# Optimization experiments

Hardware: AMD Instinct MI355X
Metric: run time of the kernel (lower is better)

Reference implementation:

```python
import jax, jax.numpy as jnp
import numpy as np

FEW, BATCH, D, STEPS = 128, 4096, 512, 4


def setup_inputs() -> dict:
    key = jax.random.key(0)
    ks = jax.random.split(key, 6)
    H = 2 * D  # LSTMCell hidden size
    return {
        "support": jax.random.normal(ks[0], (FEW, D), jnp.float32),
        "query": jax.random.normal(ks[1], (BATCH, D), jnp.float32),
        "W_ih": jax.random.normal(ks[2], (4 * H, D), jnp.float32) * (1.0 / np.sqrt(H)),
        "W_hh": jax.random.normal(ks[3], (4 * H, H), jnp.float32) * (1.0 / np.sqrt(H)),
        "b_ih": jax.random.normal(ks[4], (4 * H,), jnp.float32) * 0.01,
        "b_hh": jax.random.normal(ks[5], (4 * H,), jnp.float32) * 0.01,
        "process_step": STEPS,
    }


def reference(support, query, W_ih, W_hh, b_ih, b_hh, process_step):
    # support: (few, d); query: (batch, d); LSTMCell hidden = 2d.
    d = query.shape[1]
    batch = query.shape[0]
    h_r = jnp.zeros((batch, 2 * d), query.dtype)
    c = jnp.zeros((batch, 2 * d), query.dtype)
    h = query
    for _ in range(process_step):
        # PyTorch LSTMCell: gates ordered (i, f, g, o)
        gates = query @ W_ih.T + b_ih + h_r @ W_hh.T + b_hh  # (batch, 8d)
        i, f, g, o = jnp.split(gates, 4, axis=1)
        c = jax.nn.sigmoid(f) * c + jax.nn.sigmoid(i) * jnp.tanh(g)
        h_r_ = jax.nn.sigmoid(o) * jnp.tanh(c)  # (batch, 2d)
        h = query + h_r_[:, :d]  # (batch, d)
        attn = jax.nn.softmax(h @ support.T, axis=1)  # (batch, few)
        r = attn @ support  # (batch, d)
        h_r = jnp.concatenate([h, r], axis=1)  # (batch, 2d)
    return h
```

## Files before the change

### kernel.cpp

```cpp
#include <hip/hip_runtime.h>

#define BATCH 4096
#define DDIM  512
#define FEWN  128
#define LDA1  640
#define GATEN 2048
#define CDIM  512

typedef unsigned short ushort_t;
typedef __attribute__((ext_vector_type(8))) short bf16x8;
typedef __attribute__((ext_vector_type(4))) float f32x4;

__device__ inline ushort_t f2bf(float f) {
  unsigned u = __float_as_uint(f);
  unsigned r = (u + 0x7FFFu + ((u >> 16) & 1u)) >> 16;
  return (ushort_t)r;
}
__device__ inline float bf2f(ushort_t h) { return __uint_as_float((unsigned)h << 16); }
__device__ inline float bf2f_u(unsigned h16) { return __uint_as_float(h16 << 16); }

__device__ inline float sigmoidf(float x) { return 1.f / (1.f + __expf(-x)); }
__device__ inline float tanh_fast(float x) {
  float ax = fabsf(x);
  float t = __expf(-2.f * ax);
  float r = (1.f - t) / (1.f + t);
  return copysignf(r, x);
}

__device__ inline int orig_row(int colp) {
  return ((colp >> 4) & 3) * 1024 + ((colp >> 6) << 4) + (colp & 15);
}

__device__ inline void async_copy16(ushort_t* lds, const ushort_t* g) {
  __builtin_amdgcn_global_load_lds(
      (const __attribute__((address_space(1))) unsigned int*)g,
      (__attribute__((address_space(3))) unsigned int*)lds, 16, 0, 0);
}

#define XCD_SWZ()                                                            \
  int bx = blockIdx.x, by = blockIdx.y;                                      \
  {                                                                          \
    const int gx = gridDim.x;                                                \
    const int id = by * gx + bx;                                             \
    if ((gx & 7) == 0) {                                                     \
      const int cpx = gx >> 3;                                               \
      const int x = id & 7, s = id >> 3;                                     \
      bx = x * cpx + (s % cpx);                                              \
      by = s / cpx;                                                          \
    } else {                                                                 \
      const int nwg = gx * gridDim.y;                                        \
      const int qq = nwg >> 3, rr = nwg & 7;                                 \
      const int x = id & 7, s = id >> 3;                                     \
      const int nid = (x < rr ? x * (qq + 1) : rr * (qq + 1) + (x - rr) * qq) + s; \
      bx = nid % gx; by = nid / gx;                                          \
    }                                                                        \
  }

#define STAGE8(dA, dB, kk)                                                   \
    async_copy16(dA,              gA0 + (kk));                               \
    async_copy16(dA + 512,        gA0 + (size_t)16 * lda + (kk));            \
    async_copy16(dA + 4096,       gA0 + (kk) + 32);                          \
    async_copy16(dA + 4096 + 512, gA0 + (size_t)16 * lda + (kk) + 32);       \
    async_copy16(dB,              gB0 + (kk));                               \
    async_copy16(dB + 512,        gB0 + (size_t)16 * ldb + (kk));            \
    async_copy16(dB + 4096,       gB0 + (kk) + 32);                          \
    async_copy16(dB + 4096 + 512, gB0 + (size_t)16 * ldb + (kk) + 32);

#define KLOOP_DBUF()                                                         \
  const int nIter = K >> 6;                                                  \
  { STAGE8(sA, sB, 0) }                                                      \
  if (nIter > 1) { STAGE8(sA + 8192, sB + 8192, 64) }                        \
  for (int kt = 0; kt < nIter; ++kt) {                                       \
    if (kt + 1 < nIter) asm volatile("s_waitcnt vmcnt(8)" ::: "memory");     \
    else                asm volatile("s_waitcnt vmcnt(0)" ::: "memory");     \
    __builtin_amdgcn_s_barrier();                                            \
    const int cur = (kt & 1) * 8192;                                         \
    _Pragma("unroll")                                                        \
    for (int h = 0; h < 2; ++h) {                                            \
      bf16x8 af[4], bfr[4];                                                  \
      _Pragma("unroll")                                                      \
      for (int mi = 0; mi < 4; ++mi)                                         \
        af[mi] = *(const bf16x8*)&lA[cur + h * 4096 + (wr * 64 + mi * 16 + lr) * 32 + kg * 8]; \
      _Pragma("unroll")                                                      \
      for (int ni = 0; ni < 4; ++ni)                                         \
        bfr[ni] = *(const bf16x8*)&lB[cur + h * 4096 + (wc * 64 + ni * 16 + lr) * 32 + kg * 8]; \
      _Pragma("unroll")                                                      \
      for (int mi = 0; mi < 4; ++mi)                                         \
        _Pragma("unroll")                                                    \
        for (int ni = 0; ni < 4; ++ni)                                       \
          acc[mi][ni] = __builtin_amdgcn_mfma_f32_16x16x32_bf16(af[mi], bfr[ni], acc[mi][ni], 0, 0, 0); \
    }                                                                        \
    __builtin_amdgcn_s_barrier();                                            \
    if (kt + 2 < nIter) {                                                    \
      const int k2 = (kt + 2) << 6;                                          \
      STAGE8(sA + cur, sB + cur, k2)                                         \
    }                                                                        \
  }

#define GEMM_PROLOG()                                                        \
  __shared__ __align__(16) ushort_t lA[2 * 8192];                            \
  __shared__ __align__(16) ushort_t lB[2 * 8192];                            \
  const int tid = threadIdx.x;                                               \
  const int wid = tid >> 6, lane = tid & 63;                                 \
  const int wr = wid >> 1, wc = wid & 1;                                     \
  XCD_SWZ()                                                                  \
  const int m0 = by * 128, n0 = bx * 128;                                    \
  const int lr = lane & 15, kg = lane >> 4;                                  \
  f32x4 acc[4][4] = {};                                                      \
  const int srow = lane >> 2;                                                \
  const int scol = (lane & 3) * 8;                                           \
  const ushort_t* gA0 = A + (size_t)(m0 + wid * 32 + srow) * lda + scol;     \
  const ushort_t* gB0 = B + (size_t)(n0 + wid * 32 + srow) * ldb + scol;     \
  ushort_t* sA = &lA[wid * 1024];                                            \
  ushort_t* sB = &lB[wid * 1024];                                            \
  KLOOP_DBUF()

__launch_bounds__(256)
__global__ void gemm_wide(const ushort_t* __restrict__ A, const ushort_t* __restrict__ B,
                          ushort_t* __restrict__ gbase, ushort_t* __restrict__ c,
                          ushort_t* __restrict__ A1out, ushort_t* __restrict__ A2out,
                          const float* __restrict__ b1, const float* __restrict__ b2,
                          int K, int lda, int ldb) {
  GEMM_PROLOG()
  if (n0 < 2048) {
    const int jj = ((n0 + wc * 64) >> 6) * 16 + lr;
    const float bi0 = b1[jj]        + b2[jj];
    const float bi2 = b1[2048 + jj] + b2[2048 + jj];
    const float bi3 = b1[3072 + jj] + b2[3072 + jj];
#pragma unroll
    for (int mi = 0; mi < 4; ++mi) {
#pragma unroll
      for (int r = 0; r < 4; ++r) {
        const int row = m0 + wr * 64 + mi * 16 + kg * 4 + r;
        const float si = sigmoidf(acc[mi][0][r] + bi0);
        const float tg = tanh_fast(acc[mi][2][r] + bi2);
        const float so = sigmoidf(acc[mi][3][r] + bi3);
        const float cn = si * tg;
        c[(size_t)row * CDIM + jj] = f2bf(cn);
        const float hr = so * tanh_fast(cn);
        const ushort_t hi = f2bf(hr);
        const ushort_t lo = f2bf(hr - bf2f(hi));
        A1out[(size_t)row * LDA1 + jj] = hi;
        A2out[(size_t)row * DDIM + jj] = lo;
      }
    }
  } else {
    const int jj = ((n0 - 2048 + wc * 64) >> 6) * 16 + lr;
    const float bi0 = b1[jj]        + b2[jj];
    const float bi1 = b1[1024 + jj] + b2[1024 + jj];
    const float bi2 = b1[2048 + jj] + b2[2048 + jj];
    const float bi3 = b1[3072 + jj] + b2[3072 + jj];
#pragma unroll
    for (int mi = 0; mi < 4; ++mi)
#pragma unroll
      for (int r = 0; r < 4; ++r) {
        const int row = m0 + wr * 64 + mi * 16 + kg * 4 + r;
        uint2 p;
        p.x = (unsigned)f2bf(acc[mi][0][r] + bi0) | ((unsigned)f2bf(acc[mi][1][r] + bi1) << 16);
        p.y = (unsigned)f2bf(acc[mi][2][r] + bi2) | ((unsigned)f2bf(acc[mi][3][r] + bi3) << 16);
        *(uint2*)&gbase[(size_t)row * GATEN + jj * 4] = p;
      }
  }
}

template<int MODE>
__launch_bounds__(256)
__global__ void gemm_fused(const ushort_t* __restrict__ A, const ushort_t* __restrict__ B,
                           const ushort_t* __restrict__ base, ushort_t* __restrict__ c,
                           ushort_t* __restrict__ A1out, ushort_t* __restrict__ A2out,
                           const float* __restrict__ query, float* __restrict__ out,
                           int K, int lda, int ldb) {
  GEMM_PROLOG()
  const int jj = ((n0 + wc * 64) >> 6) * 16 + lr;
#pragma unroll
  for (int mi = 0; mi < 4; ++mi) {
#pragma unroll
    for (int r = 0; r < 4; ++r) {
      const int row = m0 + wr * 64 + mi * 16 + kg * 4 + r;
      const uint2 p = *(const uint2*)&base[(size_t)row * GATEN + jj * 4];
      const float g0 = bf2f_u(p.x & 0xFFFFu) + acc[mi][0][r];
      const float g1 = bf2f_u(p.x >> 16)     + acc[mi][1][r];
      const float g2 = bf2f_u(p.y & 0xFFFFu) + acc[mi][2][r];
      const float g3 = bf2f_u(p.y >> 16)     + acc[mi][3][r];
      const float si = sigmoidf(g0);
      const float sf = sigmoidf(g1);
      const float tg = tanh_fast(g2);
      const float so = sigmoidf(g3);
      const size_t ci = (size_t)row * CDIM + jj;
      const float cn = sf * bf2f(c[ci]) + si * tg;
      if (MODE != 2) c[ci] = f2bf(cn);
      const float hr = so * tanh_fast(cn);
      if (MODE == 2) {
        out[(size_t)row * DDIM + jj] = query[(size_t)row * DDIM + jj] + hr;
      } else {
        const ushort_t hi = f2bf(hr);
        const ushort_t lo = f2bf(hr - bf2f(hi));
        A1out[(size_t)row * LDA1 + jj] = hi;
        A2out[(size_t)row * DDIM + jj] = lo;
      }
    }
  }
}

__launch_bounds__(256)
__global__ void gemm_splitk6(const ushort_t* __restrict__ A1, const ushort_t* __restrict__ A2,
                             int lda1, int lda2,
                             const ushort_t* __restrict__ Bc, float* __restrict__ Cf) {
  __shared__ __align__(16) ushort_t lA[2 * 8192];
  __shared__ __align__(16) ushort_t lB[2 * 8192];
  const int tid = threadIdx.x;
  const int wid = tid >> 6, lane = tid & 63;
  const int wr = wid >> 1, wc = wid & 1;
  const int seg = blockIdx.x >> 1;
  const int koff = (blockIdx.x & 1) * 256;
  const int m0 = blockIdx.y * 128;
  const int lr = lane & 15, kg = lane >> 4;
  f32x4 acc[4][4] = {};
  const int srow = lane >> 2;
  const int scol = (lane & 3) * 8;
  const ushort_t* A = (seg == 1) ? A2 : A1;
  const int lda = (seg == 1) ? lda2 : lda1;
  const int ldb = 1536;
  const ushort_t* gA0 = A + (size_t)(m0 + wid * 32 + srow) * lda + koff + scol;
  const ushort_t* gB0 = Bc + (size_t)(wid * 32 + srow) * 1536 + seg * 512 + koff + scol;
  ushort_t* sA = &lA[wid * 1024];
  ushort_t* sB = &lB[wid * 1024];
  const int K = 256;
  KLOOP_DBUF()
#pragma unroll
  for (int mi = 0; mi < 4; ++mi)
#pragma unroll
    for (int ni = 0; ni < 4; ++ni)
#pragma unroll
      for (int r = 0; r < 4; ++r) {
        const int row = m0 + wr * 64 + mi * 16 + kg * 4 + r;
        const int col = wc * 64 + ni * 16 + lr;
        atomicAdd(&Cf[(size_t)row * FEWN + col], acc[mi][ni][r]);
      }
}

template<int EPI>
__launch_bounds__(256)
__global__ void gemm_bt(const ushort_t* __restrict__ A, const ushort_t* __restrict__ B,
                        float* __restrict__ Cf, ushort_t* __restrict__ Cb,
                        int K, int lda, int ldb, int ldc) {
  GEMM_PROLOG()
#pragma unroll
  for (int mi = 0; mi < 4; ++mi)
#pragma unroll
    for (int ni = 0; ni < 4; ++ni)
#pragma unroll
      for (int r = 0; r < 4; ++r) {
        const int row = m0 + wr * 64 + mi * 16 + kg * 4 + r;
        const int col = n0 + wc * 64 + ni * 16 + lr;
        const float v = acc[mi][ni][r];
        const size_t o = (size_t)row * ldc + col;
        if (EPI == 2) Cb[o] = f2bf(v);
        else          Cf[o] = v;
      }
}

__global__ void softmax_kernel(const float* __restrict__ logits, const float* __restrict__ baseL,
                               ushort_t* __restrict__ A1) {
  const int row = blockIdx.x * 4 + (threadIdx.x >> 6);
  const int lane = threadIdx.x & 63;
  const size_t ro = (size_t)row * FEWN;
  const float x0 = logits[ro + lane]      + baseL[ro + lane];
  const float x1 = logits[ro + 64 + lane] + baseL[ro + 64 + lane];
  float m = fmaxf(x0, x1);
#pragma unroll
  for (int s = 32; s > 0; s >>= 1) m = fmaxf(m, __shfl_xor(m, s));
  const float e0 = __expf(x0 - m), e1 = __expf(x1 - m);
  float sum = e0 + e1;
#pragma unroll
  for (int s = 32; s > 0; s >>= 1) sum += __shfl_xor(sum, s);
  const float inv = 1.f / sum;
  A1[(size_t)row * LDA1 + 512 + lane]      = f2bf(e0 * inv);
  A1[(size_t)row * LDA1 + 512 + 64 + lane] = f2bf(e1 * inv);
}

__global__ void setup_all(const float* __restrict__ Wih, const float* __restrict__ Whh,
                          const float* __restrict__ q, const float* __restrict__ s,
                          ushort_t* __restrict__ wcomb, ushort_t* __restrict__ B2,
                          ushort_t* __restrict__ whhRP, ushort_t* __restrict__ Q_cat,
                          ushort_t* __restrict__ B_cat) {
  const int b = blockIdx.x;
  const int tid = threadIdx.x;
  if (b < 8192) {
    const int idx = b * 256 + tid;
    const int r = idx >> 9, cc = idx & 511;
    ushort_t v;
    if (r < 2048) {
      v = f2bf(Wih[(size_t)orig_row(r) * 512 + cc]);
    } else {
      const int og = orig_row(r - 2048);
      v = f2bf(Wih[(size_t)og * 512 + cc] + Whh[(size_t)og * 1024 + cc]);
    }
    wcomb[idx] = v;
  } else if (b < 16384) {
    const int idx = (b - 8192) * 256 + tid;
    const int r = idx >> 10, k = idx & 1023;
    const ushort_t v = f2bf(Whh[(size_t)orig_row(r) * 1024 + k]);
    if (k < 512) B2[(size_t)r * LDA1 + k] = v;
    else         whhRP[(size_t)r * 512 + (k - 512)] = v;
  } else if (b < 24576) {
    const int idx = (b - 16384) * 256 + tid;
    const int bb = idx >> 9, cc = idx & 511;
    const float v = q[idx];
    const ushort_t hi = f2bf(v);
    const ushort_t lo = f2bf(v - bf2f(hi));
    const size_t ro = (size_t)bb * 1536;
    Q_cat[ro + cc] = hi;
    Q_cat[ro + 512 + cc] = lo;
    Q_cat[ro + 1024 + cc] = hi;
  } else {
    const int idx = (b - 24576) * 256 + tid;
    const int n = idx >> 9, cc = idx & 511;
    const float v = s[idx];
    const ushort_t hi = f2bf(v);
    const ushort_t lo = f2bf(v - bf2f(hi));
    const size_t ro = (size_t)n * 1536;
    B_cat[ro + cc] = hi;
    B_cat[ro + 512 + cc] = hi;
    B_cat[ro + 1024 + cc] = lo;
  }
}

extern "C" void kernel_launch(void* const* d_in, const int* in_sizes, int n_in,
                              void* d_out, int out_size, void* d_ws, size_t ws_size,
                              hipStream_t stream) {
  const float* support = (const float*)d_in[0];
  const float* query   = (const float*)d_in[1];
  const float* W_ih    = (const float*)d_in[2];
  const float* W_hh    = (const float*)d_in[3];
  const float* b_ih    = (const float*)d_in[4];
  const float* b_hh    = (const float*)d_in[5];
  float* out = (float*)d_out;

  char* ws = (char*)d_ws;
  size_t off = 0;
  auto alloc = [&](size_t bytes) { char* p = ws + off; off += (bytes + 255) & ~255ull; return p; };
  ushort_t* gates_baseP = (ushort_t*)alloc((size_t)BATCH * GATEN * 2);
  ushort_t* cbuf        = (ushort_t*)alloc((size_t)BATCH * CDIM * 2);
  ushort_t* A1a         = (ushort_t*)alloc((size_t)BATCH * LDA1 * 2);
  ushort_t* A1b         = (ushort_t*)alloc((size_t)BATCH * LDA1 * 2);
  ushort_t* A2a         = (ushort_t*)alloc((size_t)BATCH * DDIM * 2);
  ushort_t* A2b         = (ushort_t*)alloc((size_t)BATCH * DDIM * 2);
  ushort_t* Q_cat       = (ushort_t*)alloc((size_t)BATCH * 1536 * 2);
  ushort_t* wcomb       = (ushort_t*)alloc((size_t)4096 * 512 * 2);
  ushort_t* B2          = (ushort_t*)alloc((size_t)GATEN * LDA1 * 2);
  ushort_t* whhRP       = (ushort_t*)alloc((size_t)GATEN * 512 * 2);
  ushort_t* B_cat       = (ushort_t*)alloc((size_t)FEWN * 1536 * 2);
  const size_t LOFS = (size_t)BATCH * FEWN;
  float*    logits3     = (float*)   alloc(3 * LOFS * 4);
  float*    lgBase      = (float*)   alloc(LOFS * 4);
  const size_t zbytes = 4 * LOFS * 4;

  const dim3 blk(256);

  setup_all<<<24832, blk, 0, stream>>>(W_ih, W_hh, query, support,
                                       wcomb, B2, whhRP, Q_cat, B_cat);
  hipMemsetAsync(logits3, 0, zbytes, stream);

  gemm_splitk6<<<dim3(6, 32), blk, 0, stream>>>(
      Q_cat, Q_cat + 512, 1536, 1536, B_cat, lgBase);

  gemm_bt<2><<<dim3(1, 16), blk, 0, stream>>>(whhRP, B_cat, nullptr, B2 + 512,
                                              512, 512, 1536, LDA1);

  gemm_wide<<<dim3(32, 32), blk, 0, stream>>>(
      Q_cat, wcomb, gates_baseP, cbuf, A1a, A2a, b_ih, b_hh, 512, 1536, 512);

  auto attn_phase = [&](int s, ushort_t* A1, ushort_t* A2) {
    float* lg = logits3 + (size_t)s * LOFS;
    gemm_splitk6<<<dim3(6, 32), blk, 0, stream>>>(A1, A2, LDA1, DDIM, B_cat, lg);
    softmax_kernel<<<BATCH / 4, blk, 0, stream>>>(lg, lgBase, A1);
  };

  attn_phase(0, A1a, A2a);

  gemm_fused<1><<<dim3(16, 32), blk, 0, stream>>>(
      A1a, B2, gates_baseP, cbuf, A1b, A2b, nullptr, nullptr, 640, LDA1, LDA1);
  attn_phase(1, A1b, A2b);

  gemm_fused<1><<<dim3(16, 32), blk, 0, stream>>>(
      A1b, B2, gates_baseP, cbuf, A1a, A2a, nullptr, nullptr, 640, LDA1, LDA1);
  attn_phase(2, A1a, A2a);

  gemm_fused<2><<<dim3(16, 32), blk, 0, stream>>>(
      A1a, B2, gates_baseP, cbuf, nullptr, nullptr, query, out, 640, LDA1, LDA1);
}
```

Measured before the change: 189.8 us.

## Merge prologue GEMMs into one launch and fold memset into setup kernel

Three independent prologue GEMMs (base-logit split-K, W_hh·support projection, wide gate GEMM with LSTM epilogue) are combined into a single kernel that dispatches on block index, and the hipMemsetAsync zeroing of the logits buffers is moved into extra blocks of the setup kernel. This is meant to remove launch overhead and the tail-idle gaps between small kernels, letting the small GEMMs run alongside the large one. The zeroing count matches 4*LOFS floats as float4 stores. The shared macro prologue is refactored into a device helper plus a common tile macro.

```diff
diff --git a/kernel.cpp b/kernel.cpp
--- a/kernel.cpp
+++ b/kernel.cpp
@@ -37,24 +37,20 @@
       (__attribute__((address_space(3))) unsigned int*)lds, 16, 0, 0);
 }
 
-#define XCD_SWZ()                                                            \
-  int bx = blockIdx.x, by = blockIdx.y;                                      \
-  {                                                                          \
-    const int gx = gridDim.x;                                                \
-    const int id = by * gx + bx;                                             \
-    if ((gx & 7) == 0) {                                                     \
-      const int cpx = gx >> 3;                                               \
-      const int x = id & 7, s = id >> 3;                                     \
-      bx = x * cpx + (s % cpx);                                              \
-      by = s / cpx;                                                          \
-    } else {                                                                 \
-      const int nwg = gx * gridDim.y;                                        \
-      const int qq = nwg >> 3, rr = nwg & 7;                                 \
-      const int x = id & 7, s = id >> 3;                                     \
-      const int nid = (x < rr ? x * (qq + 1) : rr * (qq + 1) + (x - rr) * qq) + s; \
-      bx = nid % gx; by = nid / gx;                                          \
-    }                                                                        \
+__device__ inline void xcd_map(int gx, int gy, int id, int& bx, int& by) {
+  if ((gx & 7) == 0) {
+    const int cpx = gx >> 3;
+    const int x = id & 7, s = id >> 3;
+    bx = x * cpx + (s % cpx);
+    by = s / cpx;
+  } else {
+    const int nwg = gx * gy;
+    const int qq = nwg >> 3, rr = nwg & 7;
+    const int x = id & 7, s = id >> 3;
+    const int nid = (x < rr ? x * (qq + 1) : rr * (qq + 1) + (x - rr) * qq) + s;
+    bx = nid % gx; by = nid / gx;
   }
+}
 
 #define STAGE8(dA, dB, kk)                                                   \
     async_copy16(dA,              gA0 + (kk));                               \
@@ -97,71 +93,18 @@
     }                                                                        \
   }
 
-#define GEMM_PROLOG()                                                        \
+#define TILE_COMMON()                                                        \
   __shared__ __align__(16) ushort_t lA[2 * 8192];                            \
   __shared__ __align__(16) ushort_t lB[2 * 8192];                            \
   const int tid = threadIdx.x;                                               \
   const int wid = tid >> 6, lane = tid & 63;                                 \
   const int wr = wid >> 1, wc = wid & 1;                                     \
-  XCD_SWZ()                                                                  \
-  const int m0 = by * 128, n0 = bx * 128;                                    \
   const int lr = lane & 15, kg = lane >> 4;                                  \
-  f32x4 acc[4][4] = {};                                                      \
   const int srow = lane >> 2;                                                \
   const int scol = (lane & 3) * 8;                                           \
-  const ushort_t* gA0 = A + (size_t)(m0 + wid * 32 + srow) * lda + scol;     \
-  const ushort_t* gB0 = B + (size_t)(n0 + wid * 32 + srow) * ldb + scol;     \
+  f32x4 acc[4][4] = {};                                                      \
   ushort_t* sA = &lA[wid * 1024];                                            \
-  ushort_t* sB = &lB[wid * 1024];                                            \
-  KLOOP_DBUF()
-
-__launch_bounds__(256)
-__global__ void gemm_wide(const ushort_t* __restrict__ A, const ushort_t* __restrict__ B,
-                          ushort_t* __restrict__ gbase, ushort_t* __restrict__ c,
-                          ushort_t* __restrict__ A1out, ushort_t* __restrict__ A2out,
-                          const float* __restrict__ b1, const float* __restrict__ b2,
-                          int K, int lda, int ldb) {
-  GEMM_PROLOG()
-  if (n0 < 2048) {
-    const int jj = ((n0 + wc * 64) >> 6) * 16 + lr;
-    const float bi0 = b1[jj]        + b2[jj];
-    const float bi2 = b1[2048 + jj] + b2[2048 + jj];
-    const float bi3 = b1[3072 + jj] + b2[3072 + jj];
-#pragma unroll
-    for (int mi = 0; mi < 4; ++mi) {
-#pragma unroll
-      for (int r = 0; r < 4; ++r) {
-        const int row = m0 + wr * 64 + mi * 16 + kg * 4 + r;
-        const float si = sigmoidf(acc[mi][0][r] + bi0);
-        const float tg = tanh_fast(acc[mi][2][r] + bi2);
-        const float so = sigmoidf(acc[mi][3][r] + bi3);
-        const float cn = si * tg;
-        c[(size_t)row * CDIM + jj] = f2bf(cn);
-        const float hr = so * tanh_fast(cn);
-        const ushort_t hi = f2bf(hr);
-        const ushort_t lo = f2bf(hr - bf2f(hi));
-        A1out[(size_t)row * LDA1 + jj] = hi;
-        A2out[(size_t)row * DDIM + jj] = lo;
-      }
-    }
-  } else {
-    const int jj = ((n0 - 2048 + wc * 64) >> 6) * 16 + lr;
-    const float bi0 = b1[jj]        + b2[jj];
-    const float bi1 = b1[1024 + jj] + b2[1024 + jj];
-    const float bi2 = b1[2048 + jj] + b2[2048 + jj];
-    const float bi3 = b1[3072 + jj] + b2[3072 + jj];
-#pragma unroll
-    for (int mi = 0; mi < 4; ++mi)
-#pragma unroll
-      for (int r = 0; r < 4; ++r) {
-        const int row = m0 + wr * 64 + mi * 16 + kg * 4 + r;
-        uint2 p;
-        p.x = (unsigned)f2bf(acc[mi][0][r] + bi0) | ((unsigned)f2bf(acc[mi][1][r] + bi1) << 16);
-        p.y = (unsigned)f2bf(acc[mi][2][r] + bi2) | ((unsigned)f2bf(acc[mi][3][r] + bi3) << 16);
-        *(uint2*)&gbase[(size_t)row * GATEN + jj * 4] = p;
-      }
-  }
-}
+  ushort_t* sB = &lB[wid * 1024];
 
 template<int MODE>
 __launch_bounds__(256)
@@ -170,7 +113,13 @@
                            ushort_t* __restrict__ A1out, ushort_t* __restrict__ A2out,
                            const float* __restrict__ query, float* __restrict__ out,
                            int K, int lda, int ldb) {
-  GEMM_PROLOG()
+  TILE_COMMON()
+  int bx, by;
+  xcd_map(gridDim.x, gridDim.y, blockIdx.y * gridDim.x + blockIdx.x, bx, by);
+  const int m0 = by * 128, n0 = bx * 128;
+  const ushort_t* gA0 = A + (size_t)(m0 + wid * 32 + srow) * lda + scol;
+  const ushort_t* gB0 = B + (size_t)(n0 + wid * 32 + srow) * ldb + scol;
+  KLOOP_DBUF()
   const int jj = ((n0 + wc * 64) >> 6) * 16 + lr;
 #pragma unroll
   for (int mi = 0; mi < 4; ++mi) {
@@ -206,25 +155,15 @@
 __global__ void gemm_splitk6(const ushort_t* __restrict__ A1, const ushort_t* __restrict__ A2,
                              int lda1, int lda2,
                              const ushort_t* __restrict__ Bc, float* __restrict__ Cf) {
-  __shared__ __align__(16) ushort_t lA[2 * 8192];
-  __shared__ __align__(16) ushort_t lB[2 * 8192];
-  const int tid = threadIdx.x;
-  const int wid = tid >> 6, lane = tid & 63;
-  const int wr = wid >> 1, wc = wid & 1;
+  TILE_COMMON()
   const int seg = blockIdx.x >> 1;
   const int koff = (blockIdx.x & 1) * 256;
   const int m0 = blockIdx.y * 128;
-  const int lr = lane & 15, kg = lane >> 4;
-  f32x4 acc[4][4] = {};
-  const int srow = lane >> 2;
-  const int scol = (lane & 3) * 8;
   const ushort_t* A = (seg == 1) ? A2 : A1;
   const int lda = (seg == 1) ? lda2 : lda1;
   const int ldb = 1536;
   const ushort_t* gA0 = A + (size_t)(m0 + wid * 32 + srow) * lda + koff + scol;
   const ushort_t* gB0 = Bc + (size_t)(wid * 32 + srow) * 1536 + seg * 512 + koff + scol;
-  ushort_t* sA = &lA[wid * 1024];
-  ushort_t* sB = &lB[wid * 1024];
   const int K = 256;
   KLOOP_DBUF()
 #pragma unroll
@@ -239,25 +178,102 @@
       }
 }
 
-template<int EPI>
 __launch_bounds__(256)
-__global__ void gemm_bt(const ushort_t* __restrict__ A, const ushort_t* __restrict__ B,
-                        float* __restrict__ Cf, ushort_t* __restrict__ Cb,
-                        int K, int lda, int ldb, int ldc) {
-  GEMM_PROLOG()
-#pragma unroll
-  for (int mi = 0; mi < 4; ++mi)
-#pragma unroll
-    for (int ni = 0; ni < 4; ++ni)
-#pragma unroll
-      for (int r = 0; r < 4; ++r) {
-        const int row = m0 + wr * 64 + mi * 16 + kg * 4 + r;
-        const int col = n0 + wc * 64 + ni * 16 + lr;
-        const float v = acc[mi][ni][r];
-        const size_t o = (size_t)row * ldc + col;
-        if (EPI == 2) Cb[o] = f2bf(v);
-        else          Cf[o] = v;
+__global__ void prologue_mega(const ushort_t* __restrict__ Qcat, const ushort_t* __restrict__ Bcat,
+                              const ushort_t* __restrict__ whhRP, const ushort_t* __restrict__ wcomb,
+                              float* __restrict__ lgBase, ushort_t* __restrict__ B2,
+                              ushort_t* __restrict__ gbase, ushort_t* __restrict__ c,
+                              ushort_t* __restrict__ A1out, ushort_t* __restrict__ A2out,
+                              const float* __restrict__ b1, const float* __restrict__ b2) {
+  TILE_COMMON()
+  const int b = blockIdx.x;
+  if (b < 192) {
+    const int lbx = b % 6, lby = b / 6;
+    const int seg = lbx >> 1;
+    const int koff = (lbx & 1) * 256;
+    const int m0 = lby * 128;
+    const ushort_t* A = (seg == 1) ? Qcat + 512 : Qcat;
+    const int lda = 1536, ldb = 1536;
+    const ushort_t* gA0 = A + (size_t)(m0 + wid * 32 + srow) * lda + koff + scol;
+    const ushort_t* gB0 = Bcat + (size_t)(wid * 32 + srow) * 1536 + seg * 512 + koff + scol;
+    const int K = 256;
+    KLOOP_DBUF()
+#pragma unroll
+    for (int mi = 0; mi < 4; ++mi)
+#pragma unroll
+      for (int ni = 0; ni < 4; ++ni)
+#pragma unroll
+        for (int r = 0; r < 4; ++r) {
+          const int row = m0 + wr * 64 + mi * 16 + kg * 4 + r;
+          const int col = wc * 64 + ni * 16 + lr;
+          atomicAdd(&lgBase[(size_t)row * FEWN + col], acc[mi][ni][r]);
+        }
+  } else if (b < 208) {
+    const int m0 = (b - 192) * 128;
+    const int lda = 512, ldb = 1536;
+    const ushort_t* gA0 = whhRP + (size_t)(m0 + wid * 32 + srow) * lda + scol;
+    const ushort_t* gB0 = Bcat + (size_t)(wid * 32 + srow) * 1536 + scol;
+    const int K = 512;
+    KLOOP_DBUF()
+#pragma unroll
+    for (int mi = 0; mi < 4; ++mi)
+#pragma unroll
+      for (int ni = 0; ni < 4; ++ni)
+#pragma unroll
+        for (int r = 0; r < 4; ++r) {
+          const int row = m0 + wr * 64 + mi * 16 + kg * 4 + r;
+          const int col = wc * 64 + ni * 16 + lr;
+          B2[(size_t)row * LDA1 + 512 + col] = f2bf(acc[mi][ni][r]);
+        }
+  } else {
+    int bx, by;
+    xcd_map(32, 32, b - 208, bx, by);
+    const int m0 = by * 128, n0 = bx * 128;
+    const int lda = 1536, ldb = 512;
+    const ushort_t* gA0 = Qcat + (size_t)(m0 + wid * 32 + srow) * lda + scol;
+    const ushort_t* gB0 = wcomb + (size_t)(n0 + wid * 32 + srow) * ldb + scol;
+    const int K = 512;
+    KLOOP_DBUF()
+    if (n0 < 2048) {
+      const int jj = ((n0 + wc * 64) >> 6) * 16 + lr;
+      const float bi0 = b1[jj]        + b2[jj];
+      const float bi2 = b1[2048 + jj] + b2[2048 + jj];
+      const float bi3 = b1[3072 + jj] + b2[3072 + jj];
+#pragma unroll
+      for (int mi = 0; mi < 4; ++mi) {
+#pragma unroll
+        for (int r = 0; r < 4; ++r) {
+          const int row = m0 + wr * 64 + mi * 16 + kg * 4 + r;
+          const float si = sigmoidf(acc[mi][0][r] + bi0);
+          const float tg = tanh_fast(acc[mi][2][r] + bi2);
+          const float so = sigmoidf(acc[mi][3][r] + bi3);
+          const float cn = si * tg;
+          c[(size_t)row * CDIM + jj] = f2bf(cn);
+          const float hr = so * tanh_fast(cn);
+          const ushort_t hi = f2bf(hr);
+          const ushort_t lo = f2bf(hr - bf2f(hi));
+          A1out[(size_t)row * LDA1 + jj] = hi;
+          A2out[(size_t)row * DDIM + jj] = lo;
+        }
       }
+    } else {
+      const int jj = ((n0 - 2048 + wc * 64) >> 6) * 16 + lr;
+      const float bi0 = b1[jj]        + b2[jj];
+      const float bi1 = b1[1024 + jj] + b2[1024 + jj];
+      const float bi2 = b1[2048 + jj] + b2[2048 + jj];
+      const float bi3 = b1[3072 + jj] + b2[3072 + jj];
+#pragma unroll
+      for (int mi = 0; mi < 4; ++mi)
+#pragma unroll
+        for (int r = 0; r < 4; ++r) {
+          const int row = m0 + wr * 64 + mi * 16 + kg * 4 + r;
+          uint2 p;
+          p.x = (unsigned)f2bf(acc[mi][0][r] + bi0) | ((unsigned)f2bf(acc[mi][1][r] + bi1) << 16);
+          p.y = (unsigned)f2bf(acc[mi][2][r] + bi2) | ((unsigned)f2bf(acc[mi][3][r] + bi3) << 16);
+          *(uint2*)&gbase[(size_t)row * GATEN + jj * 4] = p;
+        }
+    }
+  }
 }
 
 __global__ void softmax_kernel(const float* __restrict__ logits, const float* __restrict__ baseL,
@@ -283,7 +299,7 @@
                           const float* __restrict__ q, const float* __restrict__ s,
                           ushort_t* __restrict__ wcomb, ushort_t* __restrict__ B2,
                           ushort_t* __restrict__ whhRP, ushort_t* __restrict__ Q_cat,
-                          ushort_t* __restrict__ B_cat) {
+                          ushort_t* __restrict__ B_cat, float4* __restrict__ zbase) {
   const int b = blockIdx.x;
   const int tid = threadIdx.x;
   if (b < 8192) {
@@ -313,7 +329,7 @@
     Q_cat[ro + cc] = hi;
     Q_cat[ro + 512 + cc] = lo;
     Q_cat[ro + 1024 + cc] = hi;
-  } else {
+  } else if (b < 24832) {
     const int idx = (b - 24576) * 256 + tid;
     const int n = idx >> 9, cc = idx & 511;
     const float v = s[idx];
@@ -323,6 +339,9 @@
     B_cat[ro + cc] = hi;
     B_cat[ro + 512 + cc] = hi;
     B_cat[ro + 1024 + cc] = lo;
+  } else {
+    const int idx = (b - 24832) * 256 + tid;
+    zbase[idx] = make_float4(0.f, 0.f, 0.f, 0.f);
   }
 }
 
@@ -354,22 +373,16 @@
   const size_t LOFS = (size_t)BATCH * FEWN;
   float*    logits3     = (float*)   alloc(3 * LOFS * 4);
   float*    lgBase      = (float*)   alloc(LOFS * 4);
-  const size_t zbytes = 4 * LOFS * 4;
 
   const dim3 blk(256);
 
-  setup_all<<<24832, blk, 0, stream>>>(W_ih, W_hh, query, support,
-                                       wcomb, B2, whhRP, Q_cat, B_cat);
-  hipMemsetAsync(logits3, 0, zbytes, stream);
-
-  gemm_splitk6<<<dim3(6, 32), blk, 0, stream>>>(
-      Q_cat, Q_cat + 512, 1536, 1536, B_cat, lgBase);
-
-  gemm_bt<2><<<dim3(1, 16), blk, 0, stream>>>(whhRP, B_cat, nullptr, B2 + 512,
-                                              512, 512, 1536, LDA1);
-
-  gemm_wide<<<dim3(32, 32), blk, 0, stream>>>(
-      Q_cat, wcomb, gates_baseP, cbuf, A1a, A2a, b_ih, b_hh, 512, 1536, 512);
+  setup_all<<<26880, blk, 0, stream>>>(W_ih, W_hh, query, support,
+                                       wcomb, B2, whhRP, Q_cat, B_cat,
+                                       (float4*)logits3);
+
+  prologue_mega<<<1232, blk, 0, stream>>>(Q_cat, B_cat, whhRP, wcomb,
+                                          lgBase, B2, gates_baseP, cbuf,
+                                          A1a, A2a, b_ih, b_hh);
 
   auto attn_phase = [&](int s, ushort_t* A1, ushort_t* A2) {
     float* lg = logits3 + (size_t)s * LOFS;
```

After: 172.1 us (median of 2 runs). 9.3% less time.
